# Performance work log

Hardware: AMD Instinct MI355X
Metric: run time of the kernel (lower is better)

Reference implementation:

```python
import jax, jax.numpy as jnp
import numpy as np
from math import ceil

N, C_IN, HV, WV = 4, 3, 256, 256
C, K, NUM_LAYERS = 16, 3, 10
HK, WK = 45, 45
PROX_SCALE, KSCALE, KBSCALE, EPS = 10.0, 100.0, 0.01, 1e-8


def conv2_same(x, w):
    # torch F.conv2d (cross-correlation) with 'same' padding
    return jax.lax.conv_general_dilated(x, w, (1, 1), 'SAME',
                                        dimension_numbers=('NCHW', 'OIHW', 'NCHW'))


def pad_to(x, size):
    h, w = x.shape[-2], x.shape[-1]
    pads = [(0, 0)] * (x.ndim - 2) + [(0, size[0] - h), (0, size[1] - w)]
    return jnp.pad(x, pads)


def soft_threshold(x, b):
    return jnp.sign(x) * jax.nn.relu(jnp.abs(x) - b)


def circ_shift(x, s):
    return jnp.roll(x, (-s[0], -s[1]), axis=(-2, -1))


def csq(c):
    return (c * jnp.conj(c)).real


def forward(blurred_image, w0, ws, biases, kernel_biases, kernel_proxes, zetas, eta):
    Nb, C_in, Hv, Wv = blurred_image.shape
    Hs, Ws = Hv + HK - 1, Wv + WK - 1
    Hb, Wb = Hs + HK - 1, Ws + WK - 1
    fft_size = (int(ceil(Hb / 64.0) * 64), int(ceil(Wb / 64.0) * 64))
    rfft = lambda x: jnp.fft.rfft2(x, s=fft_size, axes=(-2, -1))
    irfft = lambda X: jnp.fft.irfft2(X, s=fft_size, axes=(-2, -1))

    # first-layer filter: zero-mean per (out,in) filter, then spatial reflect
    w_mean = w0.reshape(C, C_in, -1).mean(axis=-1)
    w0c = w0 - w_mean[:, :, None, None]
    w0_unreflected = jnp.transpose(w0c, (1, 0, 2, 3))   # (C_in, C, K, K)
    w0r = w0c[:, :, ::-1, ::-1]

    # analysis: cascade of convs, each feature stack padded to fft_size
    wy_list = []
    fy = blurred_image
    for layer in range(NUM_LAYERS):
        w = w0r if layer == 0 else ws[layer - 1]
        fy = conv2_same(fy, w)
        fy_p = pad_to(jnp.pad(fy, ((0, 0), (0, 0), (HK - 1, HK - 1), (WK - 1, WK - 1))), fft_size)
        wy_list.append(fy_p)

    delta = jnp.zeros((Nb, HK, WK), dtype=blurred_image.dtype).at[:, HK // 2, WK // 2].set(1.0)
    b0 = biases[0][None, :, None, None]
    z = soft_threshold(circ_shift(wy_list[-1], (HK // 2, WK // 2)), b0)
    Fz = rfft(z)
    k = delta
    Fg = None
    for layer in range(NUM_LAYERS):
        fy_p = wy_list.pop()
        Ffy = rfft(fy_p)                       # (N, C, H, Wf) complex
        Fk = rfft(k)[:, None]                  # (N, 1, H, Wf)
        zeta = PROX_SCALE * zetas[layer][None, :, None, None]
        num = zeta * (jnp.conj(Fk) * Ffy) + Fz
        den = zeta * csq(Fk) + 1.0
        Fg = num / (den + EPS)
        b = biases[layer + 1][None, :, None, None]
        z = soft_threshold(irfft(Fg), b)
        Fz = rfft(z)
        zk = kernel_proxes[layer]
        num_k = zk * jnp.sum(jnp.conj(Fz) * Ffy, axis=1) + Fk[:, 0]
        den_k = zk * jnp.sum(csq(Fz), axis=1) + 1.0
        k = irfft(num_k / (den_k + EPS))
        k_flat = k.reshape(Nb, -1)
        k_max = jax.scipy.special.logsumexp(k_flat * KSCALE, axis=-1) / KSCALE
        bk = KBSCALE * kernel_biases[layer]
        k = jax.nn.relu(k[:, :HK, :WK] - bk * k_max[:, None, None])
        k_sum = jnp.sum(k, axis=(1, 2), keepdims=True)
        k = (k + EPS * delta) / (k_sum + EPS)

    # final closed-form image solve in frequency domain (3-channel Cramer's rule)
    Fy = rfft(jnp.pad(blurred_image, ((0, 0), (0, 0), (HK - 1, HK - 1), (WK - 1, WK - 1))))
    Fk = rfft(k)                                # (N, H, Wf)
    Fw0 = rfft(circ_shift(pad_to(w0_unreflected, fft_size), (K // 2, K // 2)))  # (C_in, C, H, Wf)
    b_final = biases[NUM_LAYERS + 1][None, :, None, None]
    Fg = rfft(soft_threshold(irfft(Fg), b_final))

    eta_s = PROX_SCALE * eta[None, :, None, None]      # (1, C, 1, 1)
    Fwr, Fwg, Fwb = Fw0[0:1], Fw0[1:2], Fw0[2:3]       # (1, C, H, Wf)
    Fyr, Fyg, Fyb = Fy[:, 0], Fy[:, 1], Fy[:, 2]
    Fk_sq = csq(Fk)
    Crr = Fk_sq + jnp.sum(eta_s * csq(Fwr), axis=1)
    Cgg = Fk_sq + jnp.sum(eta_s * csq(Fwg), axis=1)
    Cbb = Fk_sq + jnp.sum(eta_s * csq(Fwb), axis=1)
    Crg = jnp.sum(eta_s * jnp.conj(Fwr) * Fwg, axis=1)
    Crb = jnp.sum(eta_s * jnp.conj(Fwr) * Fwb, axis=1)
    Cgb = jnp.sum(eta_s * jnp.conj(Fwg) * Fwb, axis=1)
    Fk_conj = jnp.conj(Fk)
    Br = Fk_conj * Fyr + jnp.sum(eta_s * jnp.conj(Fwr) * Fg, axis=1)
    Bg = Fk_conj * Fyg + jnp.sum(eta_s * jnp.conj(Fwg) * Fg, axis=1)
    Bb = Fk_conj * Fyb + jnp.sum(eta_s * jnp.conj(Fwb) * Fg, axis=1)
    Crg_sq, Crb_sq, Cgb_sq = csq(Crg), csq(Crb), csq(Cgb)
    Irr = Cgg * Cbb - Cgb_sq
    Igg = Crr * Cbb - Crb_sq
    Ibb = Crr * Cgg - Crg_sq
    Irg = jnp.conj(Cgb) * Crb - Cbb * Crg
    Irb = Crg * Cgb - Cgg * Crb
    Igb = jnp.conj(Crg) * Crb - Crr * Cgb
    den = (Crr * (Cgg * Cbb - Cgb_sq) - Cgg * Crb_sq - Cbb * Crg_sq
           + 2 * (Crg * Cgb * jnp.conj(Crb)).real) + EPS
    Fxr = Irr * Br + Irg * Bg + Irb * Bb
    Fxg = jnp.conj(Irg) * Br + Igg * Bg + Igb * Bb
    Fxb = jnp.conj(Irb) * Br + jnp.conj(Igb) * Bg + Ibb * Bb
    Fx = jnp.stack([Fxr, Fxg, Fxb], axis=1) / den[:, None]

    image = irfft(Fx)[:, :, HK // 2:HK // 2 + Hv, WK // 2:WK // 2 + Wv]
    return image, k


def setup_inputs() -> dict:
    key = jax.random.key(0)
    ks = jax.random.split(key, 4)

    def xavier(k, shape, fan_in, fan_out):
        std = (2.0 / (fan_in + fan_out)) ** 0.5
        return std * jax.random.normal(k, shape, dtype=jnp.float32)

    return {
        'blurred_image': jax.random.normal(ks[0], (N, C_IN, HV, WV), dtype=jnp.float32),
        'w0': xavier(ks[1], (C, C_IN, K, K), C_IN * K * K, C * K * K),
        'ws': xavier(ks[2], (NUM_LAYERS - 1, C, C, 3, 3), C * 9, C * 9),
        'biases': jnp.full((NUM_LAYERS + 2, C), 0.02, dtype=jnp.float32),
        'kernel_biases': jnp.zeros((NUM_LAYERS,), dtype=jnp.float32),
        'kernel_proxes': jnp.ones((NUM_LAYERS,), dtype=jnp.float32),
        'zetas': jnp.ones((NUM_LAYERS, C), dtype=jnp.float32),
        'eta': jnp.ones((C,), dtype=jnp.float32),
    }


def reference(blurred_image, w0, ws, biases, kernel_biases, kernel_proxes, zetas, eta):
    return forward(blurred_image, w0, ws, biases, kernel_biases, kernel_proxes, zetas, eta)
```

## Files before the change

kernel.cpp:

```cpp
#include <hip/hip_runtime.h>
#include <math.h>

#define FH 384
#define KF 193
#define SPW 147456

typedef __attribute__((ext_vector_type(8))) short short8;
typedef __attribute__((ext_vector_type(4))) float f32x4;
typedef unsigned int u32;
typedef unsigned short u16;

static __device__ __forceinline__ float softt(float v, float b) {
    return copysignf(fmaxf(fabsf(v) - b, 0.f), v);
}
static __device__ __forceinline__ u16 bf16_rn(float v) {
    u32 u = __float_as_uint(v);
    u32 r = (u + 0x7FFFu + ((u >> 16) & 1u)) >> 16;
    return (u16)r;
}
static __device__ __forceinline__ float bf16_to_f(u16 h) {
    return __uint_as_float(((u32)h) << 16);
}
static __device__ __forceinline__ float2 ldc(const uint2* __restrict__ S, size_t i) {
    uint2 u = S[i];
    float2 r;
    r.x = __uint_as_float((u.x & 0xffffu) << 16) + __uint_as_float((u.y & 0xffffu) << 16);
    r.y = __uint_as_float(u.x & 0xffff0000u) + __uint_as_float(u.y & 0xffff0000u);
    return r;
}
static __device__ __forceinline__ float2 ldcu(uint2 u) {
    float2 r;
    r.x = __uint_as_float((u.x & 0xffffu) << 16) + __uint_as_float((u.y & 0xffffu) << 16);
    r.y = __uint_as_float(u.x & 0xffff0000u) + __uint_as_float(u.y & 0xffff0000u);
    return r;
}
static __device__ __forceinline__ uint2 packc(float re, float im) {
    u16 hr = bf16_rn(re), hi = bf16_rn(im);
    u16 lr = bf16_rn(re - bf16_to_f(hr)), li = bf16_rn(im - bf16_to_f(hi));
    uint2 o; o.x = (u32)hr | ((u32)hi << 16); o.y = (u32)lr | ((u32)li << 16);
    return o;
}
static __device__ __forceinline__ float2 cmul(float2 a, float2 b) {
    float2 r; r.x = a.x*b.x - a.y*b.y; r.y = a.x*b.y + a.y*b.x; return r;
}

__global__ void init_ef_k(float2* Ef) {
    int idx = blockIdx.x * 256 + threadIdx.x;
    if (idx >= FH * FH) return;
    int h = idx / FH, j = idx % FH;
    int m = (h * j) % FH;
    float th = (float)(6.283185307179586 / FH) * (float)m;
    float2 v; v.x = cosf(th); v.y = -sinf(th);
    Ef[idx] = v;
}

__global__ void init_tw(float2* twT) {
    int i = blockIdx.x * 256 + threadIdx.x;
    if (i < 384) {
        float th = (float)(6.283185307179586 / 384.0) * (float)i;
        float2 v; v.x = cosf(th); v.y = sinf(th);
        twT[i] = v;
    }
}

__global__ void init_e48(u16* __restrict__ H, u16* __restrict__ L, int inv)
{
    int idx = blockIdx.x * 256 + threadIdx.x;
    if (idx >= 96 * 96) return;
    int gm = idx / 96, kp = idx % 96;
    int m = gm >> 1, comp = gm & 1;
    int t = kp >> 1, ri = kp & 1;
    int mm = (m * t) % 48;
    float th = (float)(6.283185307179586 / 48.0) * (float)mm;
    float c = cosf(th), s = sinf(th);
    float er, ei;
    if (inv) { er = c * (1.f/384.f); ei = s * (1.f/384.f); }
    else     { er = c;               ei = -s; }
    float v;
    if (comp == 0) v = (ri == 0) ? er : -ei;
    else           v = (ri == 0) ? ei :  er;
    u16 h = bf16_rn(v);
    H[idx] = h;
    L[idx] = bf16_rn(v - bf16_to_f(h));
}

__global__ void init_t192(u16* __restrict__ H, u16* __restrict__ L)
{
    int idx = blockIdx.x * 256 + threadIdx.x;
    if (idx >= 208 * 192) return;
    int n = idx / 192, m = idx % 192;
    float v = 0.f;
    if (n < 194) {
        int j = n >> 1, ri = n & 1;
        int mm = (j * m) % 192;
        float th = (float)(6.283185307179586 / 192.0) * (float)mm;
        v = ri ? -sinf(th) : cosf(th);
    }
    u16 h = bf16_rn(v);
    H[idx] = h;
    L[idx] = bf16_rn(v - bf16_to_f(h));
}

__global__ void init_u192(u16* __restrict__ H, u16* __restrict__ L)
{
    int idx = blockIdx.x * 256 + threadIdx.x;
    if (idx >= 192 * 224) return;
    int m = idx / 224, kk = idx % 224;
    float v = 0.f;
    if (kk < 194) {
        int j = kk >> 1, ri = kk & 1;
        float cj = (j == 0 || j == 96) ? (1.f/384.f) : (2.f/384.f);
        int mm = (j * m) % 192;
        float th = (float)(6.283185307179586 / 192.0) * (float)mm;
        v = ri ? -cj*sinf(th) : cj*cosf(th);
    }
    u16 h = bf16_rn(v);
    H[idx] = h;
    L[idx] = bf16_rn(v - bf16_to_f(h));
}

__global__ void w0c_kernel(const float* __restrict__ w0, float* __restrict__ w0c) {
    int t = threadIdx.x;
    if (t < 48) {
        float m = 0.f;
        for (int d = 0; d < 9; ++d) m += w0[t*9+d];
        m *= (1.f/9.f);
        for (int d = 0; d < 9; ++d) w0c[t*9+d] = w0[t*9+d] - m;
    }
}

__global__ __launch_bounds__(256) void conv3x3_kernel(
    const float* __restrict__ inpF0, const u16* __restrict__ inH0, const u16* __restrict__ inL0,
    const float* __restrict__ w,
    u16* __restrict__ outH0, u16* __restrict__ outL0, int Cin, int flip,
    size_t inImgStride)
{
    size_t iofs = (size_t)blockIdx.z * inImgStride;
    const float* inF = inpF0 ? inpF0 + iofs : nullptr;
    const u16*   iH  = inH0 ? inH0 + iofs : nullptr;
    const u16*   iL  = inL0 ? inL0 + iofs : nullptr;
    u16* oH = outH0 + (size_t)blockIdx.z * 16*65536;
    u16* oL = outL0 + (size_t)blockIdx.z * 16*65536;
    __shared__ float tile[18][19];
    __shared__ float wl[16*16*9];
    int x0 = blockIdx.x * 16, y0 = blockIdx.y * 16;
    int t = threadIdx.x;
    int tx = t & 15, ty = t >> 4;
    int nw = 16 * Cin * 9;
    for (int i = t; i < nw; i += 256) {
        int d = i % 9;
        wl[i] = flip ? w[i + 8 - 2*d] : w[i];
    }
    float acc[16];
#pragma unroll
    for (int co = 0; co < 16; ++co) acc[co] = 0.f;
    for (int ci = 0; ci < Cin; ++ci) {
        __syncthreads();
        for (int i = t; i < 18*18; i += 256) {
            int yy = i / 18, xx = i % 18;
            int gy = y0 - 1 + yy, gx = x0 - 1 + xx;
            float v = 0.f;
            if (gy >= 0 && gy < 256 && gx >= 0 && gx < 256) {
                size_t ii;
                if (inF) ii = ((size_t)ci*256 + gy)*256 + gx;
                else     ii = ((size_t)ci*256 + gy)*256 + ((gx>>1) + (gx&1)*128);
                v = inF ? inF[ii] : (bf16_to_f(iH[ii]) + bf16_to_f(iL[ii]));
            }
            tile[yy][xx] = v;
        }
        __syncthreads();
        float v[9];
#pragma unroll
        for (int dy = 0; dy < 3; dy++)
#pragma unroll
            for (int dx = 0; dx < 3; dx++) v[dy*3+dx] = tile[ty+dy][tx+dx];
#pragma unroll
        for (int co = 0; co < 16; co++) {
            const float* wp = &wl[(co*Cin+ci)*9];
            acc[co] += v[0]*wp[0]+v[1]*wp[1]+v[2]*wp[2]
                     + v[3]*wp[3]+v[4]*wp[4]+v[5]*wp[5]
                     + v[6]*wp[6]+v[7]*wp[7]+v[8]*wp[8];
        }
    }
    int xo = x0 + tx;
    int xd = (xo >> 1) + (xo & 1)*128;
#pragma unroll
    for (int co = 0; co < 16; co++) {
        size_t o = ((size_t)co*256 + (y0+ty))*256 + xd;
        u16 h = bf16_rn(acc[co]);
        oH[o] = h;
        oL[o] = bf16_rn(acc[co] - bf16_to_f(h));
    }
}

__global__ void zinit_kernel(const u16* __restrict__ fy9H, const u16* __restrict__ fy9L,
                             const float* __restrict__ b0,
// ... 259 lines not shown
{
    int idx = blockIdx.x*256 + threadIdx.x;
    if (idx >= rows * 97) return;
    int j = idx % 97;
    size_t b = (size_t)(idx / 97) * KF;
    if (j == 96) {
        float2 f = ldc(S, b + 96);
        S[b + 96] = packc(2.f*f.x, -2.f*f.y);
    } else {
        float2 f1 = ldc(S, b + j);
        float2 f2 = ldc(S, b + 192 - j);
        float gpx = f1.x + f2.x, gpy = f1.y - f2.y;
        float hx  = f1.x - f2.x, hy  = f1.y + f2.y;
        float2 tw = twT[j];
        float gmx = tw.x*hx - tw.y*hy;
        float gmy = tw.x*hy + tw.y*hx;
        S[b + j]       = packc(gpx, gpy);
        S[b + 192 - j] = packc(gmx, gmy);
    }
}

template<bool FUSE_LSE>
__global__ __launch_bounds__(256) void c2r192(
    const uint2* __restrict__ Ain,
    const u16* __restrict__ UH, const u16* __restrict__ UL,
    float* __restrict__ outp, const float* __restrict__ thr,
    u16* __restrict__ spH, u16* __restrict__ spL, int B,
    float2* __restrict__ parts)
{
    __shared__ u16 AhS[2][8*64*8];
    __shared__ u16 AlS[2][8*64*8];
    int col0 = blockIdx.x * 64;
    int y0   = blockIdx.y * 128;
    int plane = blockIdx.z;
    int tid = threadIdx.x;
    int wave = tid >> 6, lane = tid & 63;
    int lm = lane & 15, lq = lane >> 4;
    f32x4 accP[2][4], accQ[2][4];
#pragma unroll
    for (int mi = 0; mi < 2; ++mi)
#pragma unroll
        for (int nj = 0; nj < 4; ++nj) {
            accP[mi][nj] = (f32x4){0.f,0.f,0.f,0.f};
            accQ[mi][nj] = (f32x4){0.f,0.f,0.f,0.f};
        }
    for (int kt = 0; kt < 194; kt += 32) {
#pragma unroll
        for (int s = 0; s < 8; ++s) {
            int slot = tid + s*256;
            int p   = slot >> 10;
            int inr = slot & 1023;
            int r = inr >> 3, kq = inr & 7;
            size_t rowb = ((size_t)(y0 + r)*B + plane)*KF;
            int j0 = (kt + kq*4) >> 1;
            uint2 u0, u1;
            u0.x = u0.y = u1.x = u1.y = 0u;
            if (p == 0) {
                if (j0 < 96) u0 = Ain[rowb + j0];
                else if (j0 == 96) {
                    uint2 t = Ain[rowb + 96];
                    u0.x = t.x & 0xffffu; u0.y = t.y & 0xffffu;
                }
                if (j0 + 1 < 96) u1 = Ain[rowb + j0 + 1];
            } else {
                if (j0 < 96) u0 = Ain[rowb + 192 - j0];
                else if (j0 == 96) {
                    uint2 t = Ain[rowb + 96];
                    u0.x = t.x >> 16; u0.y = t.y >> 16;
                }
                if (j0 + 1 < 96) u1 = Ain[rowb + 191 - j0];
            }
            int base = ((r >> 4)*64 + (r & 15) + 16*(kq >> 1))*8 + (kq & 1)*4;
            uint2 hp, lp;
            hp.x = u0.x; hp.y = u1.x;
            lp.x = u0.y; lp.y = u1.y;
            *(uint2*)&AhS[p][base] = hp;
            *(uint2*)&AlS[p][base] = lp;
        }
        __syncthreads();
        short8 A0h[2], A0l[2], A1h[2], A1l[2];
#pragma unroll
        for (int mi = 0; mi < 2; ++mi) {
            int fo = ((wave*2 + mi)*64 + lane)*8;
            A0h[mi] = *(const short8*)&AhS[0][fo];
            A0l[mi] = *(const short8*)&AlS[0][fo];
            A1h[mi] = *(const short8*)&AhS[1][fo];
            A1l[mi] = *(const short8*)&AlS[1][fo];
        }
#pragma unroll
        for (int nj = 0; nj < 4; ++nj) {
            size_t toff = (size_t)(col0 + nj*16 + lm)*224 + kt + lq*8;
            short8 Bh = *(const short8*)(UH + toff);
            short8 Bl = *(const short8*)(UL + toff);
#pragma unroll
            for (int mi = 0; mi < 2; ++mi) {
                accP[mi][nj] = __builtin_amdgcn_mfma_f32_16x16x32_bf16(A0h[mi], Bh, accP[mi][nj], 0, 0, 0);
                accP[mi][nj] = __builtin_amdgcn_mfma_f32_16x16x32_bf16(A0h[mi], Bl, accP[mi][nj], 0, 0, 0);
                accP[mi][nj] = __builtin_amdgcn_mfma_f32_16x16x32_bf16(A0l[mi], Bh, accP[mi][nj], 0, 0, 0);
                accQ[mi][nj] = __builtin_amdgcn_mfma_f32_16x16x32_bf16(A1h[mi], Bh, accQ[mi][nj], 0, 0, 0);
                accQ[mi][nj] = __builtin_amdgcn_mfma_f32_16x16x32_bf16(A1h[mi], Bl, accQ[mi][nj], 0, 0, 0);
                accQ[mi][nj] = __builtin_amdgcn_mfma_f32_16x16x32_bf16(A1l[mi], Bh, accQ[mi][nj], 0, 0, 0);
            }
        }
        __syncthreads();
    }
    float bthr = thr ? thr[plane & 15] : 0.f;
    float lm_ = -1e30f, ls_ = 0.f;
#pragma unroll
    for (int mi = 0; mi < 2; ++mi) {
#pragma unroll
        for (int nj = 0; nj < 4; ++nj) {
            int m = col0 + nj*16 + lm;
#pragma unroll
            for (int rr = 0; rr < 4; ++rr) {
                int y = y0 + wave*32 + mi*16 + lq*4 + rr;
                float xe = accP[mi][nj][rr];
                float xo = accQ[mi][nj][rr];
                float2 o2; o2.x = xe; o2.y = xo;
                *(float2*)&outp[((size_t)plane*FH + y)*FH + 2*m] = o2;
                if (spH) {
                    float s0 = softt(xe, bthr), s1 = softt(xo, bthr);
                    u16 h0 = bf16_rn(s0), h1 = bf16_rn(s1);
                    u16 l0 = bf16_rn(s0 - bf16_to_f(h0)), l1 = bf16_rn(s1 - bf16_to_f(h1));
                    size_t d = (size_t)plane*SPW + (size_t)y*FH + m;
                    spH[d]       = h0; spL[d]       = l0;
                    spH[d + 192] = h1; spL[d + 192] = l1;
                }
                if (FUSE_LSE) {
                    lse_comb(lm_, ls_, 100.f*xe, 1.f);
                    lse_comb(lm_, ls_, 100.f*xo, 1.f);
                }
            }
        }
    }
    if (FUSE_LSE) {
        __shared__ float sm[256], ss[256];
        sm[tid] = lm_; ss[tid] = ls_;
        __syncthreads();
        for (int st = 128; st > 0; st >>= 1) {
            if (tid < st) {
                float mm = sm[tid], sc = ss[tid];
                lse_comb(mm, sc, sm[tid+st], ss[tid+st]);
                sm[tid] = mm; ss[tid] = sc;
            }
            __syncthreads();
        }
        if (tid == 0) {
            float2 o; o.x = sm[0]; o.y = ss[0];
            parts[plane*9 + blockIdx.y*3 + blockIdx.x] = o;
        }
    }
}

template<bool FUSE_FG>
__global__ __launch_bounds__(384) void zgemm_col_mfma8(
    const u16* __restrict__ EH, const u16* __restrict__ EL,
    const uint2* __restrict__ Bm, uint2* __restrict__ Cm, int N, float sgn,
    int ktHi, const float2* __restrict__ twT,
    uint2* __restrict__ FzFg, const uint2* __restrict__ FkB,
    const float* __restrict__ zet16, int GKF)
{
    __shared__ u16 BhS[8][2*64*8];
    __shared__ u16 BlS[8][2*64*8];
    int col0 = blockIdx.x * 32;
    int tid = threadIdx.x;
    int wave = tid >> 6, lane = tid & 63;
    int lm = lane & 15, lq = lane >> 4;
    f32x4 acc[8][2];
#pragma unroll
    for (int p = 0; p < 8; ++p)
#pragma unroll
        for (int nj = 0; nj < 2; ++nj)
            acc[p][nj] = (f32x4){0.f,0.f,0.f,0.f};
    int arow = wave*16 + lm;
    for (int kt = 0; kt < ktHi; kt += 32) {
        int tbase = kt >> 1;
#pragma unroll
        for (int s = 0; s < 6; ++s) {
            int slot = tid + s*384;
            if (slot < 2048) {
                int p    = slot >> 8;
                int inr  = slot & 255;
                int pair = inr >> 5;
                int n    = inr & 31;
                int gn   = col0 + n;
                int t0   = tbase + pair*2;
                uint2 u0, u1;
                u0.x = u0.y = u1.x = u1.y = 0u;
                if (gn < N) {
                    u0 = Bm[(size_t)(8*t0 + p)*N + gn];
                    u1 = Bm[(size_t)(8*t0 + 8 + p)*N + gn];
                }
                int ntile = n >> 4, n0 = n & 15;
                int lrow  = (pair >> 1)*16 + n0;
                int base  = (ntile*64 + lrow)*8 + (pair & 1)*4;
                uint2 hp, lp;
                hp.x = u0.x; hp.y = u1.x;
                lp.x = u0.y; lp.y = u1.y;
                *(uint2*)&BhS[p][base] = hp;
                *(uint2*)&BlS[p][base] = lp;
            }
        }
        __syncthreads();
        short8 Ah, Al;
        {
            size_t aoff = (size_t)arow*96 + kt + lq*8;
            Ah = *(const short8*)(EH + aoff);
            Al = *(const short8*)(EL + aoff);
        }
#pragma unroll
        for (int nj = 0; nj < 2; ++nj) {
#pragma unroll
            for (int p = 0; p < 8; ++p) {
                short8 Bh = *(const short8*)&BhS[p][(nj*64 + lane)*8];
                short8 Bl = *(const short8*)&BlS[p][(nj*64 + lane)*8];
                acc[p][nj] = __builtin_amdgcn_mfma_f32_16x16x32_bf16(Ah, Bh, acc[p][nj], 0, 0, 0);
                acc[p][nj] = __builtin_amdgcn_mfma_f32_16x16x32_bf16(Ah, Bl, acc[p][nj], 0, 0, 0);
                acc[p][nj] = __builtin_amdgcn_mfma_f32_16x16x32_bf16(Al, Bh, acc[p][nj], 0, 0, 0);
            }
        }
        __syncthreads();
    }
    const float rt = 0.70710678118654752f;
#pragma unroll
    for (int nj = 0; nj < 2; ++nj) {
        int coln = col0 + nj*16 + lm;
        if (coln < N) {
            int r0 = wave*16 + lq*4;
            int h0b = r0 >> 1;
            int kk = 0, imgI = 0;
            float zeta = 0.f;
            if (FUSE_FG) {
                int planeI = coln / KF;
                kk = coln - planeI*KF;
                imgI = planeI >> 4;
                zeta = 10.f * zet16[planeI & 15];
            }
#pragma unroll
            for (int pp = 0; pp < 2; ++pp) {
                int h0 = h0b + pp;
                float2 d[8];
                d[0].x = acc[0][nj][2*pp]; d[0].y = acc[0][nj][2*pp+1];
#pragma unroll
                for (int p = 1; p < 8; ++p) {
                    float2 w = twT[p*h0];
                    w.y *= sgn;
                    float2 c; c.x = acc[p][nj][2*pp]; c.y = acc[p][nj][2*pp+1];
                    d[p] = cmul(c, w);
                }
                float2 e0, e1, e2, e3, o0, o1, o2, o3;
                e0.x = d[0].x + d[4].x; e0.y = d[0].y + d[4].y;
                e1.x = d[1].x + d[5].x; e1.y = d[1].y + d[5].y;
                e2.x = d[2].x + d[6].x; e2.y = d[2].y + d[6].y;
                e3.x = d[3].x + d[7].x; e3.y = d[3].y + d[7].y;
                o0.x = d[0].x - d[4].x; o0.y = d[0].y - d[4].y;
                o1.x = d[1].x - d[5].x; o1.y = d[1].y - d[5].y;
                o2.x = d[2].x - d[6].x; o2.y = d[2].y - d[6].y;
                o3.x = d[3].x - d[7].x; o3.y = d[3].y - d[7].y;
                float2 s02, m02, s13, m13, i13;
                s02.x = e0.x + e2.x; s02.y = e0.y + e2.y;
                m02.x = e0.x - e2.x; m02.y = e0.y - e2.y;
                s13.x = e1.x + e3.x; s13.y = e1.y + e3.y;
                m13.x = e1.x - e3.x; m13.y = e1.y - e3.y;
                i13.x = -sgn*m13.y;  i13.y = sgn*m13.x;
                float2 X[8];
                X[0].x = s02.x + s13.x; X[0].y = s02.y + s13.y;
                X[4].x = s02.x - s13.x; X[4].y = s02.y - s13.y;
                X[2].x = m02.x + i13.x; X[2].y = m02.y + i13.y;
                X[6].x = m02.x - i13.x; X[6].y = m02.y - i13.y;
                float2 g0 = o0, g1, g2, g3;
                g1.x = rt*(o1.x - sgn*o1.y);  g1.y = rt*(sgn*o1.x + o1.y);
                g2.x = -sgn*o2.y;             g2.y = sgn*o2.x;
                g3.x = rt*(-(o3.x + sgn*o3.y)); g3.y = rt*(sgn*o3.x - o3.y);
                float2 sp, mp, sq, mq, iq;
                sp.x = g0.x + g2.x; sp.y = g0.y + g2.y;
                mp.x = g0.x - g2.x; mp.y = g0.y - g2.y;
                sq.x = g1.x + g3.x; sq.y = g1.y + g3.y;
                mq.x = g1.x - g3.x; mq.y = g1.y - g3.y;
                iq.x = -sgn*mq.y;   iq.y = sgn*mq.x;
                X[1].x = sp.x + sq.x; X[1].y = sp.y + sq.y;
                X[5].x = sp.x - sq.x; X[5].y = sp.y - sq.y;
                X[3].x = mp.x + iq.x; X[3].y = mp.y + iq.y;
                X[7].x = mp.x - iq.x; X[7].y = mp.y - iq.y;
#pragma unroll
                for (int q = 0; q < 8; ++q) {
                    int row = h0 + 48*q;
                    uint2 px = packc(X[q].x, X[q].y);
                    Cm[(size_t)row*N + coln] = px;
                    if (FUSE_FG) {
                        float2 fy = ldcu(px);
                        float2 fz = ldc(FzFg, (size_t)row*N + coln);
                        float2 fk = ldc(FkB, (size_t)row*GKF + imgI*KF + kk);
                        float nx = zeta*(fk.x*fy.x + fk.y*fy.y) + fz.x;
                        float ny = zeta*(fk.x*fy.y - fk.y*fy.x) + fz.y;
                        float den = zeta*(fk.x*fk.x + fk.y*fk.y) + 1.f + 1e-8f;
                        float inv = 1.f/den;
                        FzFg[(size_t)row*N + coln] = packc(nx*inv, ny*inv);
                    }
                }
            }
        }
    }
}

__global__ void knum_kernel(const uint2* __restrict__ Fz, const uint2* __restrict__ Ffy,
                            const uint2* __restrict__ Fk, const float* __restrict__ kprox,
                            int L, int total, uint2* __restrict__ outk)
{
    int idx = blockIdx.x*256 + threadIdx.x;
    if (idx >= total) return;
    int k = idx % KF; int r = idx / KF;
    float zk = kprox[L];
    float s1x = 0.f, s1y = 0.f, s2 = 0.f;
    for (int c = 0; c < 16; ++c) {
        size_t bi = ((size_t)r*16 + c)*KF + k;
        float2 fz = ldc(Fz, bi), fy = ldc(Ffy, bi);
        s1x += fz.x*fy.x + fz.y*fy.y;
        s1y += fz.x*fy.y - fz.y*fy.x;
        s2  += fz.x*fz.x + fz.y*fz.y;
    }
    float2 fk = ldc(Fk, idx);
    float nx = zk*s1x + fk.x, ny = zk*s1y + fk.y;
    float den = zk*s2 + 1.f + 1e-8f;
    float inv = 1.f/den;
    outk[idx] = packc(nx*inv, ny*inv);
}

__global__ void zero_kernel(float* __restrict__ p, int n)
{
    int i = blockIdx.x*256 + threadIdx.x;
    if (i < n) p[i] = 0.f;
}

__global__ void kdelta_kernel(float* __restrict__ kful, int G)
{
    int t = threadIdx.x;
    if (t < G) kful[(size_t)t*FH*FH + 22*FH + 22] = 1.f;
}

__global__ __launch_bounds__(256) void knew_kernel(const float2* __restrict__ parts,
    const float* __restrict__ kraw0, const float* __restrict__ kb, int L,
    float* __restrict__ kful0)
{
    int img = blockIdx.x;
    const float* kraw = kraw0 + (size_t)img*FH*FH;
    float*       kful = kful0 + (size_t)img*FH*FH;
    int t = threadIdx.x;
    __shared__ float sm[16], ss[16];
    if (t < 16) {
        if (t < 9) { float2 p = parts[img*9 + t]; sm[t] = p.x; ss[t] = p.y; }
        else       { sm[t] = -1e30f; ss[t] = 0.f; }
    }
    __syncthreads();
    for (int st = 8; st > 0; st >>= 1) {
        if (t < st) {
            float mm = sm[t], sc = ss[t];
            lse_comb(mm, sc, sm[t+st], ss[t+st]);
            sm[t] = mm; ss[t] = sc;
        }
        __syncthreads();
    }
    float kmax = (sm[0] + logf(ss[0])) * 0.01f;
    float thr = 0.01f * kb[L] * kmax;
    float vs[8]; float loc = 0.f;
#pragma unroll
    for (int ii = 0; ii < 8; ++ii) {
        int i = t + ii*256;
        float v = 0.f;
        if (i < 45*45) {
            int y = i/45, x = i - y*45;
            v = fmaxf(kraw[y*FH + x] - thr, 0.f);
        }
        vs[ii] = v; loc += v;
    }
    __shared__ float sr[256];
    sr[t] = loc; __syncthreads();
    for (int st = 128; st > 0; st >>= 1) { if (t < st) sr[t] += sr[t+st]; __syncthreads(); }
    float den = sr[0] + 1e-8f;
#pragma unroll
    for (int ii = 0; ii < 8; ++ii) {
        int i = t + ii*256;
        if (i < 45*45) {
            int y = i/45, x = i - y*45;
            float v = vs[ii] + ((y == 22 && x == 22) ? 1e-8f : 0.f);
            kful[y*FH + x] = v / den;
        }
    }
}

__global__ void fw0_kernel(const float* __restrict__ w0c, const float2* __restrict__ Ef,
                           float2* __restrict__ Fw0)
{
    int idx = blockIdx.x*256 + threadIdx.x;
    if (idx >= 48*FH*KF) return;
    int k = idx % KF; int r = idx / KF;
    int c = r & 15; int r2 = r >> 4;
    int ci = r2 % 3; int h = r2 / 3;
    float accx = 0.f, accy = 0.f;
#pragma unroll
    for (int ky = 0; ky < 3; ++ky) {
        int a1 = ky - 1; if (a1 < 0) a1 += FH;
        float2 e1 = Ef[h*FH + a1];
#pragma unroll
        for (int kx = 0; kx < 3; ++kx) {
            int a2 = kx - 1; if (a2 < 0) a2 += FH;
            float2 e2 = Ef[k*FH + a2];
            float wv = w0c[((c*3 + ci)*3 + ky)*3 + kx];
            float tr = e1.x*e2.x - e1.y*e2.y;
            float ti = e1.x*e2.y + e1.y*e2.x;
            accx += wv*tr; accy += wv*ti;
        }
    }
    float2 o; o.x = accx; o.y = accy;
    Fw0[idx] = o;
}

__global__ void wiener_kernel(const uint2* __restrict__ Fk, const uint2* __restrict__ Fy,
    const float2* __restrict__ Fw0, const uint2* __restrict__ Fg2,
    const float* __restrict__ eta, int G, int total, uint2* __restrict__ Fx)
{
    int idx = blockIdx.x*256 + threadIdx.x;
    if (idx >= total) return;
    int k = idx % KF; int r = idx / KF;
    int h = r / G;
    float2 fk = ldc(Fk, idx);
    float fksq = fk.x*fk.x + fk.y*fk.y;
    float2 fyr = ldc(Fy, ((size_t)3*r + 0)*KF + k);
    float2 fyg = ldc(Fy, ((size_t)3*r + 1)*KF + k);
    float2 fyb = ldc(Fy, ((size_t)3*r + 2)*KF + k);
    float Crr = fksq, Cgg = fksq, Cbb = fksq;
    float2 Crg, Crb, Cgb;
    Crg.x = Crg.y = Crb.x = Crb.y = Cgb.x = Cgb.y = 0.f;
    float2 Br, Bg, Bb;
    Br.x = fk.x*fyr.x + fk.y*fyr.y; Br.y = fk.x*fyr.y - fk.y*fyr.x;
    Bg.x = fk.x*fyg.x + fk.y*fyg.y; Bg.y = fk.x*fyg.y - fk.y*fyg.x;
    Bb.x = fk.x*fyb.x + fk.y*fyb.y; Bb.y = fk.x*fyb.y - fk.y*fyb.x;
    for (int c = 0; c < 16; ++c) {
        float es = 10.f * eta[c];
        float2 wr = Fw0[((size_t)h*48 +  0 + c)*KF + k];
        float2 wg = Fw0[((size_t)h*48 + 16 + c)*KF + k];
        float2 wb = Fw0[((size_t)h*48 + 32 + c)*KF + k];
        float2 g  = ldc(Fg2, ((size_t)r*16 + c)*KF + k);
        Crr += es*(wr.x*wr.x + wr.y*wr.y);
        Cgg += es*(wg.x*wg.x + wg.y*wg.y);
        Cbb += es*(wb.x*wb.x + wb.y*wb.y);
        Crg.x += es*(wr.x*wg.x + wr.y*wg.y); Crg.y += es*(wr.x*wg.y - wr.y*wg.x);
        Crb.x += es*(wr.x*wb.x + wr.y*wb.y); Crb.y += es*(wr.x*wb.y - wr.y*wb.x);
        Cgb.x += es*(wg.x*wb.x + wg.y*wb.y); Cgb.y += es*(wg.x*wb.y - wg.y*wb.x);
        Br.x += es*(wr.x*g.x + wr.y*g.y); Br.y += es*(wr.x*g.y - wr.y*g.x);
        Bg.x += es*(wg.x*g.x + wg.y*g.y); Bg.y += es*(wg.x*g.y - wg.y*g.x);
        Bb.x += es*(wb.x*g.x + wb.y*g.y); Bb.y += es*(wb.x*g.y - wb.y*g.x);
    }
    float Crg_sq = Crg.x*Crg.x + Crg.y*Crg.y;
    float Crb_sq = Crb.x*Crb.x + Crb.y*Crb.y;
    float Cgb_sq = Cgb.x*Cgb.x + Cgb.y*Cgb.y;
    float Irr = Cgg*Cbb - Cgb_sq;
    float Igg = Crr*Cbb - Crb_sq;
    float Ibb = Crr*Cgg - Crg_sq;
    float2 Irg, Irb, Igb;
    Irg.x = (Cgb.x*Crb.x + Cgb.y*Crb.y) - Cbb*Crg.x;
    Irg.y = (Cgb.x*Crb.y - Cgb.y*Crb.x) - Cbb*Crg.y;
    Irb.x = (Crg.x*Cgb.x - Crg.y*Cgb.y) - Cgg*Crb.x;
    Irb.y = (Crg.x*Cgb.y + Crg.y*Cgb.x) - Cgg*Crb.y;
    Igb.x = (Crg.x*Crb.x + Crg.y*Crb.y) - Crr*Cgb.x;
    Igb.y = (Crg.x*Crb.y - Crg.y*Crb.x) - Crr*Cgb.y;
    float tx_ = Crg.x*Cgb.x - Crg.y*Cgb.y;
    float ty_ = Crg.x*Cgb.y + Crg.y*Cgb.x;
    float den = Crr*Irr - Cgg*Crb_sq - Cbb*Crg_sq + 2.f*(tx_*Crb.x + ty_*Crb.y) + 1e-8f;
    float inv = 1.f/den;
    float ox, oy;
    ox = (Irr*Br.x + (Irg.x*Bg.x - Irg.y*Bg.y) + (Irb.x*Bb.x - Irb.y*Bb.y))*inv;
    oy = (Irr*Br.y + (Irg.x*Bg.y + Irg.y*Bg.x) + (Irb.x*Bb.y + Irb.y*Bb.x))*inv;
    Fx[((size_t)3*r + 0)*KF + k] = packc(ox, oy);
    ox = ((Irg.x*Br.x + Irg.y*Br.y) + Igg*Bg.x + (Igb.x*Bb.x - Igb.y*Bb.y))*inv;
    oy = ((Irg.x*Br.y - Irg.y*Br.x) + Igg*Bg.y + (Igb.x*Bb.y + Igb.y*Bb.x))*inv;
    Fx[((size_t)3*r + 1)*KF + k] = packc(ox, oy);
    ox = ((Irb.x*Br.x + Irb.y*Br.y) + (Igb.x*Bg.x + Igb.y*Bg.y) + Ibb*Bb.x)*inv;
    oy = ((Irb.x*Br.y - Irb.y*Br.x) + (Igb.x*Bg.y - Igb.y*Bg.x) + Ibb*Bb.y)*inv;
    Fx[((size_t)3*r + 2)*KF + k] = packc(ox, oy);
}

__global__ void crop_kernel(const float* __restrict__ sp, float* __restrict__ outp, int total)
{
    int idx = blockIdx.x*256 + threadIdx.x;
    if (idx >= total) return;
    int x = idx & 255; int r = idx >> 8; int y = r & 255; int plane = r >> 8;
    outp[idx] = sp[((size_t)plane*FH + (y+22))*FH + (x+22)];
}

__global__ void kcopy_kernel(const float* __restrict__ kful, float* __restrict__ outp, int total)
{
    int idx = blockIdx.x*256 + threadIdx.x;
    if (idx >= total) return;
    int rem = idx % 2025; int img = idx / 2025;
    int x = rem % 45; int y = rem / 45;
    outp[idx] = kful[(size_t)img*FH*FH + y*FH + x];
}

extern "C" void kernel_launch(void* const* d_in, const int* in_sizes, int n_in,
                              void* d_out, int out_size, void* d_ws, size_t ws_size,
                              hipStream_t stream)
{
    (void)in_sizes; (void)n_in; (void)out_size;
    const float* blurred = (const float*)d_in[0];
    const float* w0      = (const float*)d_in[1];
    const float* wsw     = (const float*)d_in[2];
    const float* biases  = (const float*)d_in[3];
    const float* kbias   = (const float*)d_in[4];
    const float* kprox   = (const float*)d_in[5];
    const float* zetas   = (const float*)d_in[6];
    const float* eta     = (const float*)d_in[7];
    float* outp = (float*)d_out;

    auto al = [](size_t b) { return (b + 255) & ~(size_t)255; };
    auto need = [&](int G) -> size_t {
        size_t s = 0;
        s += al((size_t)FH*FH*8);
        s += al(384*8);
        s += 4*al((size_t)96*96*2);
        s += 2*al((size_t)208*192*2);
        s += 2*al((size_t)192*224*2);
        s += al(432*4);
        s += 2*al((size_t)10*G*16*65536*2);
        s += al((size_t)G*16*FH*FH*4);
        s += 2*al((size_t)G*16*SPW*2);
        s += 3*al((size_t)G*16*FH*KF*8);
        s += 4*al((size_t)G*FH*KF*8);
        s += 2*al((size_t)G*FH*FH*4);
        s += 2*al((size_t)G*3*FH*KF*8);
        s += al((size_t)G*64*8);
        return s;
    };
    int G = 4;
    while (G > 1 && need(G) > ws_size) G >>= 1;

    char* base = (char*)d_ws;
    size_t off = 0;
    auto alloc = [&](size_t bytes) -> void* {
        void* p = (void*)(base + off);
        off += (bytes + 255) & ~(size_t)255;
        return p;
    };
    float2* Ef   = (float2*)alloc((size_t)FH*FH*8);
    float2* twT  = (float2*)alloc(384*8);
    u16* EfH = (u16*)alloc((size_t)96*96*2);
    u16* EfL = (u16*)alloc((size_t)96*96*2);
    u16* EiH = (u16*)alloc((size_t)96*96*2);
    u16* EiL = (u16*)alloc((size_t)96*96*2);
    u16* T1H = (u16*)alloc((size_t)208*192*2);
    u16* T1L = (u16*)alloc((size_t)208*192*2);
    u16* U1H = (u16*)alloc((size_t)192*224*2);
    u16* U1L = (u16*)alloc((size_t)192*224*2);
    float*  w0cB = (float*)alloc(432*4);
    u16*    fyH  = (u16*)alloc((size_t)10*G*16*65536*2);
    u16*    fyL  = (u16*)alloc((size_t)10*G*16*65536*2);
    float*  zsp  = (float*)alloc((size_t)G*16*FH*FH*4);
    u16*    zspSH= (u16*)alloc((size_t)G*16*SPW*2);
    u16*    zspSL= (u16*)alloc((size_t)G*16*SPW*2);
    uint2*  mid  = (uint2*)alloc((size_t)G*16*FH*KF*8);
    uint2*  FzFg = (uint2*)alloc((size_t)G*16*FH*KF*8);
    uint2*  Ffy  = (uint2*)alloc((size_t)G*16*FH*KF*8);
    uint2*  Fk   = (uint2*)alloc((size_t)G*FH*KF*8);
    uint2*  kfA  = (uint2*)alloc((size_t)G*FH*KF*8);
    uint2*  kfB  = (uint2*)alloc((size_t)G*FH*KF*8);
    uint2*  kmid = (uint2*)alloc((size_t)G*FH*KF*8);
    float*  kraw = (float*)alloc((size_t)G*FH*FH*4);
    float*  kful = (float*)alloc((size_t)G*FH*FH*4);
    uint2*  FyB  = (uint2*)alloc((size_t)G*3*FH*KF*8);
    uint2*  FxB  = (uint2*)alloc((size_t)G*3*FH*KF*8);
    float2* lseP = (float2*)alloc((size_t)G*64*8);
    float2* Fw0B = (float2*)fyH;

    init_ef_k<<<(FH*FH+255)/256, 256, 0, stream>>>(Ef);
    init_tw<<<2, 256, 0, stream>>>(twT);
    init_e48<<<(96*96+255)/256, 256, 0, stream>>>(EfH, EfL, 0);
    init_e48<<<(96*96+255)/256, 256, 0, stream>>>(EiH, EiL, 1);
    init_t192<<<(208*192+255)/256, 256, 0, stream>>>(T1H, T1L);
    init_u192<<<(192*224+255)/256, 256, 0, stream>>>(U1H, U1L);
    w0c_kernel<<<1, 64, 0, stream>>>(w0, w0cB);

    auto zgf = [&](const uint2* Bm, uint2* Cm, int Ncols) {
        zgemm_col_mfma8<false><<<dim3((Ncols+31)/32), 384, 0, stream>>>(
            EfH, EfL, Bm, Cm, Ncols, -1.f, 96, twT, nullptr, nullptr, nullptr, 0);
    };
    auto zgi = [&](const uint2* Bm, uint2* Cm, int Ncols) {
        zgemm_col_mfma8<false><<<dim3((Ncols+31)/32), 384, 0, stream>>>(
            EiH, EiL, Bm, Cm, Ncols, 1.f, 96, twT, nullptr, nullptr, nullptr, 0);
    };
    auto r2c = [&](const float* inp, int inH, int inW, int oY, int oX,
                   const float* thr, uint2* o, int B) {
        r2c192_f<<<dim3(4, 3, B), 256, 0, stream>>>(
            inp, inH, inW, inW, (size_t)inH*inW, oY, oX, thr, T1H, T1L, twT, o, B);
    };
    auto r2cs = [&](const u16* Hs, const u16* Ls, int inH, int inW, int oY, int oX,
                    uint2* o, int B) {
        r2c192_s<<<dim3(4, 3, B), 256, 0, stream>>>(
            Hs, Ls, inH, inW, oY, oX, T1H, T1L, twT, o, B);
    };
    auto c2r = [&](uint2* Ain, float* o, int B,
                   const float* thr, u16* sH, u16* sL) {
        int rows = FH * B;
        gpm_kernel<<<(rows*97 + 255)/256, 256, 0, stream>>>(Ain, twT, rows);
        c2r192<false><<<dim3(3, 3, B), 256, 0, stream>>>(
            Ain, U1H, U1L, o, thr, sH, sL, B, nullptr);
    };
    auto c2rk = [&](uint2* Ain, float* o, int B, float2* parts) {
        int rows = FH * B;
        gpm_kernel<<<(rows*97 + 255)/256, 256, 0, stream>>>(Ain, twT, rows);
        c2r192<true><<<dim3(3, 3, B), 256, 0, stream>>>(
            Ain, U1H, U1L, o, nullptr, nullptr, nullptr, B, parts);
    };
    auto r2ck = [&]() {
        r2c192_f<<<dim3(4, 1, G), 256, 0, stream>>>(
            kful, 45, 45, FH, (size_t)FH*FH, 0, 0, nullptr, T1H, T1L, twT, kmid, G);
        zgemm_col_mfma8<false><<<dim3((G*KF+31)/32), 384, 0, stream>>>(
            EfH, EfL, kmid, Fk, G*KF, -1.f, 32, twT, nullptr, nullptr, nullptr, 0);
    };

    const size_t CKL = (size_t)G*16*65536;

    for (int g0 = 0; g0 < 4; g0 += G) {
        const float* img = blurred + (size_t)g0*3*65536;

        conv3x3_kernel<<<dim3(16,16,G), 256, 0, stream>>>(
            img, nullptr, nullptr, w0cB, fyH, fyL, 3, 1, (size_t)3*65536);
        for (int l = 1; l < 10; ++l)
            conv3x3_kernel<<<dim3(16,16,G), 256, 0, stream>>>(
                nullptr, fyH + (size_t)(l-1)*CKL, fyL + (size_t)(l-1)*CKL,
                wsw + (size_t)(l-1)*2304,
                fyH + (size_t)l*CKL, fyL + (size_t)l*CKL, 16, 0, (size_t)16*65536);

        int totZ = G*16*FH*FH;
        zinit_kernel<<<(totZ+255)/256, 256, 0, stream>>>(
            fyH + 9*CKL, fyL + 9*CKL, biases, zspSH, zspSL, totZ);
        r2cs(zspSH, zspSL, FH, FH, 0, 0, mid, G*16);
        zgf(mid, FzFg, G*16*KF);

        zero_kernel<<<(G*FH*FH+255)/256, 256, 0, stream>>>(kful, G*FH*FH);
        kdelta_kernel<<<1, 64, 0, stream>>>(kful, G);

        int totK = G*FH*KF;
        int NS = G*16*KF;
        for (int it = 0; it < 10; ++it) {
            int Lfy = 9 - it;
            r2ck();
            r2cs(fyH + (size_t)Lfy*CKL, fyL + (size_t)Lfy*CKL, 256, 256, 44, 44, mid, G*16);
            zgemm_col_mfma8<true><<<dim3((NS+31)/32), 384, 0, stream>>>(
                EfH, EfL, mid, Ffy, NS, -1.f, 96, twT,
                FzFg, Fk, zetas + it*16, G*KF);
            zgi(FzFg, mid, NS);
            c2r(mid, zsp, G*16, biases + (it+1)*16, zspSH, zspSL);
            r2cs(zspSH, zspSL, FH, FH, 0, 0, mid, G*16);
            zgf(mid, FzFg, NS);
            knum_kernel<<<(totK+255)/256, 256, 0, stream>>>(FzFg, Ffy, Fk, kprox, it, totK, kfA);
            zgi(kfA, kfB, G*KF);
            c2rk(kfB, kraw, G, lseP);
            knew_kernel<<<G, 256, 0, stream>>>(lseP, kraw, kbias, it, kful);
        }

        r2c(img, 256, 256, 44, 44, nullptr, mid, 3*G);
        zgf(mid, FyB, 3*G*KF);
        r2ck();
        r2c(zsp, FH, FH, 0, 0, biases + 11*16, mid, G*16);
        zgf(mid, FzFg, G*16*KF);
        fw0_kernel<<<(48*FH*KF+255)/256, 256, 0, stream>>>(w0cB, Ef, Fw0B);
        wiener_kernel<<<(totK+255)/256, 256, 0, stream>>>(Fk, FyB, Fw0B, FzFg, eta, G, totK, FxB);
        zgi(FxB, mid, 3*G*KF);
        c2r(mid, zsp, 3*G, nullptr, nullptr, nullptr);
        int totC = G*3*65536;
        crop_kernel<<<(totC+255)/256, 256, 0, stream>>>(zsp, outp + (size_t)g0*3*65536, totC);
        int totKC = G*2025;
        kcopy_kernel<<<(totKC+255)/256, 256, 0, stream>>>(kful, outp + 786432 + g0*2025, totKC);
    }
}
```

Baseline: 7.612 ms.

## Fuse forward column DFT, Fg update and inverse column DFT into one kernel

Adds zgemm_fg_inv, which performs the forward column DFT GEMM, computes the Fg proximal update in registers, and then runs the inverse column DFT GEMM on that result using shared memory. No intermediate FzFg write and reread or separate inverse launch is needed. This removes one kernel launch and a full round trip of the spectrum through global memory in each of the 10 iterations. The cost is extra register pressure from holding packed results (pg) plus a second accumulator set, which may lower occupancy. The butterfly is factored into a helper, bfly8.

```diff
diff --git a/kernel.cpp b/kernel.cpp
--- a/kernel.cpp
+++ b/kernel.cpp
@@ -42,6 +42,53 @@
 }
 static __device__ __forceinline__ float2 cmul(float2 a, float2 b) {
     float2 r; r.x = a.x*b.x - a.y*b.y; r.y = a.x*b.y + a.y*b.x; return r;
+}
+
+static __device__ __forceinline__ void bfly8(const float2 cc[8], int h0, float sgn,
+                                             const float2* __restrict__ twT, float2 X[8])
+{
+    const float rt = 0.70710678118654752f;
+    float2 d[8];
+    d[0] = cc[0];
+#pragma unroll
+    for (int p = 1; p < 8; ++p) {
+        float2 w = twT[p*h0];
+        w.y *= sgn;
+        d[p] = cmul(cc[p], w);
+    }
+    float2 e0, e1, e2, e3, o0, o1, o2, o3;
+    e0.x = d[0].x + d[4].x; e0.y = d[0].y + d[4].y;
+    e1.x = d[1].x + d[5].x; e1.y = d[1].y + d[5].y;
+    e2.x = d[2].x + d[6].x; e2.y = d[2].y + d[6].y;
+    e3.x = d[3].x + d[7].x; e3.y = d[3].y + d[7].y;
+    o0.x = d[0].x - d[4].x; o0.y = d[0].y - d[4].y;
+    o1.x = d[1].x - d[5].x; o1.y = d[1].y - d[5].y;
+    o2.x = d[2].x - d[6].x; o2.y = d[2].y - d[6].y;
+    o3.x = d[3].x - d[7].x; o3.y = d[3].y - d[7].y;
+    float2 s02, m02, s13, m13, i13;
+    s02.x = e0.x + e2.x; s02.y = e0.y + e2.y;
+    m02.x = e0.x - e2.x; m02.y = e0.y - e2.y;
+    s13.x = e1.x + e3.x; s13.y = e1.y + e3.y;
+    m13.x = e1.x - e3.x; m13.y = e1.y - e3.y;
+    i13.x = -sgn*m13.y;  i13.y = sgn*m13.x;
+    X[0].x = s02.x + s13.x; X[0].y = s02.y + s13.y;
+    X[4].x = s02.x - s13.x; X[4].y = s02.y - s13.y;
+    X[2].x = m02.x + i13.x; X[2].y = m02.y + i13.y;
+    X[6].x = m02.x - i13.x; X[6].y = m02.y - i13.y;
+    float2 g0 = o0, g1, g2, g3;
+    g1.x = rt*(o1.x - sgn*o1.y);  g1.y = rt*(sgn*o1.x + o1.y);
+    g2.x = -sgn*o2.y;             g2.y = sgn*o2.x;
+    g3.x = rt*(-(o3.x + sgn*o3.y)); g3.y = rt*(sgn*o3.x - o3.y);
+    float2 sp, mp, sq, mq, iq;
+    sp.x = g0.x + g2.x; sp.y = g0.y + g2.y;
+    mp.x = g0.x - g2.x; mp.y = g0.y - g2.y;
+    sq.x = g1.x + g3.x; sq.y = g1.y + g3.y;
+    mq.x = g1.x - g3.x; mq.y = g1.y - g3.y;
+    iq.x = -sgn*mq.y;   iq.y = sgn*mq.x;
+    X[1].x = sp.x + sq.x; X[1].y = sp.y + sq.y;
+    X[5].x = sp.x - sq.x; X[5].y = sp.y - sq.y;
+    X[3].x = mp.x + iq.x; X[3].y = mp.y + iq.y;
+    X[7].x = mp.x - iq.x; X[7].y = mp.y - iq.y;
 }
 
 __global__ void init_ef_k(float2* Ef) {
@@ -607,13 +654,10 @@
     }
 }
 
-template<bool FUSE_FG>
 __global__ __launch_bounds__(384) void zgemm_col_mfma8(
     const u16* __restrict__ EH, const u16* __restrict__ EL,
     const uint2* __restrict__ Bm, uint2* __restrict__ Cm, int N, float sgn,
-    int ktHi, const float2* __restrict__ twT,
-    uint2* __restrict__ FzFg, const uint2* __restrict__ FkB,
-    const float* __restrict__ zet16, int GKF)
+    int ktHi, const float2* __restrict__ twT)
 {
     __shared__ u16 BhS[8][2*64*8];
     __shared__ u16 BlS[8][2*64*8];
@@ -676,82 +720,210 @@
         }
         __syncthreads();
     }
-    const float rt = 0.70710678118654752f;
 #pragma unroll
     for (int nj = 0; nj < 2; ++nj) {
         int coln = col0 + nj*16 + lm;
         if (coln < N) {
             int r0 = wave*16 + lq*4;
             int h0b = r0 >> 1;
-            int kk = 0, imgI = 0;
-            float zeta = 0.f;
-            if (FUSE_FG) {
-                int planeI = coln / KF;
-                kk = coln - planeI*KF;
-                imgI = planeI >> 4;
-                zeta = 10.f * zet16[planeI & 15];
-            }
 #pragma unroll
             for (int pp = 0; pp < 2; ++pp) {
                 int h0 = h0b + pp;
-                float2 d[8];
-                d[0].x = acc[0][nj][2*pp]; d[0].y = acc[0][nj][2*pp+1];
-#pragma unroll
-                for (int p = 1; p < 8; ++p) {
-                    float2 w = twT[p*h0];
-                    w.y *= sgn;
-                    float2 c; c.x = acc[p][nj][2*pp]; c.y = acc[p][nj][2*pp+1];
-                    d[p] = cmul(c, w);
-                }
-                float2 e0, e1, e2, e3, o0, o1, o2, o3;
-                e0.x = d[0].x + d[4].x; e0.y = d[0].y + d[4].y;
-                e1.x = d[1].x + d[5].x; e1.y = d[1].y + d[5].y;
-                e2.x = d[2].x + d[6].x; e2.y = d[2].y + d[6].y;
-                e3.x = d[3].x + d[7].x; e3.y = d[3].y + d[7].y;
-                o0.x = d[0].x - d[4].x; o0.y = d[0].y - d[4].y;
-                o1.x = d[1].x - d[5].x; o1.y = d[1].y - d[5].y;
-                o2.x = d[2].x - d[6].x; o2.y = d[2].y - d[6].y;
-                o3.x = d[3].x - d[7].x; o3.y = d[3].y - d[7].y;
-                float2 s02, m02, s13, m13, i13;
-                s02.x = e0.x + e2.x; s02.y = e0.y + e2.y;
-                m02.x = e0.x - e2.x; m02.y = e0.y - e2.y;
-                s13.x = e1.x + e3.x; s13.y = e1.y + e3.y;
-                m13.x = e1.x - e3.x; m13.y = e1.y - e3.y;
-                i13.x = -sgn*m13.y;  i13.y = sgn*m13.x;
+                float2 cc[8];
+#pragma unroll
+                for (int p = 0; p < 8; ++p) {
+                    cc[p].x = acc[p][nj][2*pp]; cc[p].y = acc[p][nj][2*pp+1];
+                }
                 float2 X[8];
-                X[0].x = s02.x + s13.x; X[0].y = s02.y + s13.y;
-                X[4].x = s02.x - s13.x; X[4].y = s02.y - s13.y;
-                X[2].x = m02.x + i13.x; X[2].y = m02.y + i13.y;
-                X[6].x = m02.x - i13.x; X[6].y = m02.y - i13.y;
-                float2 g0 = o0, g1, g2, g3;
-                g1.x = rt*(o1.x - sgn*o1.y);  g1.y = rt*(sgn*o1.x + o1.y);
-                g2.x = -sgn*o2.y;             g2.y = sgn*o2.x;
-                g3.x = rt*(-(o3.x + sgn*o3.y)); g3.y = rt*(sgn*o3.x - o3.y);
-                float2 sp, mp, sq, mq, iq;
-                sp.x = g0.x + g2.x; sp.y = g0.y + g2.y;
-                mp.x = g0.x - g2.x; mp.y = g0.y - g2.y;
-                sq.x = g1.x + g3.x; sq.y = g1.y + g3.y;
-                mq.x = g1.x - g3.x; mq.y = g1.y - g3.y;
-                iq.x = -sgn*mq.y;   iq.y = sgn*mq.x;
-                X[1].x = sp.x + sq.x; X[1].y = sp.y + sq.y;
-                X[5].x = sp.x - sq.x; X[5].y = sp.y - sq.y;
-                X[3].x = mp.x + iq.x; X[3].y = mp.y + iq.y;
-                X[7].x = mp.x - iq.x; X[7].y = mp.y - iq.y;
+                bfly8(cc, h0, sgn, twT, X);
+#pragma unroll
+                for (int q = 0; q < 8; ++q) {
+                    int row = h0 + 48*q;
+                    Cm[(size_t)row*N + coln] = packc(X[q].x, X[q].y);
+                }
+            }
+        }
+    }
+}
+
+__global__ __launch_bounds__(384) void zgemm_fg_inv(
+    const u16* __restrict__ EH, const u16* __restrict__ EL,
+    const u16* __restrict__ IH, const u16* __restrict__ IL,
+    uint2* __restrict__ Bm, uint2* __restrict__ Ffy,
+    const uint2* __restrict__ FzB, const uint2* __restrict__ FkB,
+    const float* __restrict__ zet16, int N, int GKF,
+    const float2* __restrict__ twT)
+{
+    __shared__ u16 BhS[8][2*64*8];
+    __shared__ u16 BlS[8][2*64*8];
+    int col0 = blockIdx.x * 32;
+    int tid = threadIdx.x;
+    int wave = tid >> 6, lane = tid & 63;
+    int lm = lane & 15, lq = lane >> 4;
+    int arow = wave*16 + lm;
+    f32x4 acc[8][2];
+#pragma unroll
+    for (int p = 0; p < 8; ++p)
+#pragma unroll
+        for (int nj = 0; nj < 2; ++nj)
+            acc[p][nj] = (f32x4){0.f,0.f,0.f,0.f};
+    for (int kt = 0; kt < 96; kt += 32) {
+        int tbase = kt >> 1;
+#pragma unroll
+        for (int s = 0; s < 6; ++s) {
+            int slot = tid + s*384;
+            if (slot < 2048) {
+                int p    = slot >> 8;
+                int inr  = slot & 255;
+                int pair = inr >> 5;
+                int n    = inr & 31;
+                int gn   = col0 + n;
+                int t0   = tbase + pair*2;
+                uint2 u0, u1;
+                u0.x = u0.y = u1.x = u1.y = 0u;
+                if (gn < N) {
+                    u0 = Bm[(size_t)(8*t0 + p)*N + gn];
+                    u1 = Bm[(size_t)(8*t0 + 8 + p)*N + gn];
+                }
+                int ntile = n >> 4, n0 = n & 15;
+                int lrow  = (pair >> 1)*16 + n0;
+                int base  = (ntile*64 + lrow)*8 + (pair & 1)*4;
+                uint2 hp, lp;
+                hp.x = u0.x; hp.y = u1.x;
+                lp.x = u0.y; lp.y = u1.y;
+                *(uint2*)&BhS[p][base] = hp;
+                *(uint2*)&BlS[p][base] = lp;
+            }
+        }
+        __syncthreads();
+        short8 Ah, Al;
+        {
+            size_t aoff = (size_t)arow*96 + kt + lq*8;
+            Ah = *(const short8*)(EH + aoff);
+            Al = *(const short8*)(EL + aoff);
+        }
+#pragma unroll
+        for (int nj = 0; nj < 2; ++nj) {
+#pragma unroll
+            for (int p = 0; p < 8; ++p) {
+                short8 Bh = *(const short8*)&BhS[p][(nj*64 + lane)*8];
+                short8 Bl = *(const short8*)&BlS[p][(nj*64 + lane)*8];
+                acc[p][nj] = __builtin_amdgcn_mfma_f32_16x16x32_bf16(Ah, Bh, acc[p][nj], 0, 0, 0);
+                acc[p][nj] = __builtin_amdgcn_mfma_f32_16x16x32_bf16(Ah, Bl, acc[p][nj], 0, 0, 0);
+                acc[p][nj] = __builtin_amdgcn_mfma_f32_16x16x32_bf16(Al, Bh, acc[p][nj], 0, 0, 0);
+            }
+        }
+        __syncthreads();
+    }
+    int r0 = wave*16 + lq*4;
+    int h0b = r0 >> 1;
+    uint2 pg[2][2][8];
+#pragma unroll
+    for (int nj = 0; nj < 2; ++nj)
+#pragma unroll
+        for (int pp = 0; pp < 2; ++pp)
+#pragma unroll
+            for (int q = 0; q < 8; ++q) { pg[nj][pp][q].x = 0u; pg[nj][pp][q].y = 0u; }
+#pragma unroll
+    for (int nj = 0; nj < 2; ++nj) {
+        int coln = col0 + nj*16 + lm;
+        if (coln < N) {
+            int planeI = coln / KF;
+            int kk = coln - planeI*KF;
+            int imgI = planeI >> 4;
+            float zeta = 10.f * zet16[planeI & 15];
+#pragma unroll
+            for (int pp = 0; pp < 2; ++pp) {
+                int h0 = h0b + pp;
+                float2 cc[8];
+#pragma unroll
+                for (int p = 0; p < 8; ++p) {
+                    cc[p].x = acc[p][nj][2*pp]; cc[p].y = acc[p][nj][2*pp+1];
+                }
+                float2 X[8];
+                bfly8(cc, h0, -1.f, twT, X);
 #pragma unroll
                 for (int q = 0; q < 8; ++q) {
                     int row = h0 + 48*q;
                     uint2 px = packc(X[q].x, X[q].y);
-                    Cm[(size_t)row*N + coln] = px;
-                    if (FUSE_FG) {
-                        float2 fy = ldcu(px);
-                        float2 fz = ldc(FzFg, (size_t)row*N + coln);
-                        float2 fk = ldc(FkB, (size_t)row*GKF + imgI*KF + kk);
-                        float nx = zeta*(fk.x*fy.x + fk.y*fy.y) + fz.x;
-                        float ny = zeta*(fk.x*fy.y - fk.y*fy.x) + fz.y;
-                        float den = zeta*(fk.x*fk.x + fk.y*fk.y) + 1.f + 1e-8f;
-                        float inv = 1.f/den;
-                        FzFg[(size_t)row*N + coln] = packc(nx*inv, ny*inv);
+                    Ffy[(size_t)row*N + coln] = px;
+                    float2 fy = ldcu(px);
+                    float2 fz = ldc(FzB, (size_t)row*N + coln);
+                    float2 fk = ldc(FkB, (size_t)row*GKF + imgI*KF + kk);
+                    float nx = zeta*(fk.x*fy.x + fk.y*fy.y) + fz.x;
+                    float ny = zeta*(fk.x*fy.y - fk.y*fy.x) + fz.y;
+                    float den = zeta*(fk.x*fk.x + fk.y*fk.y) + 1.f + 1e-8f;
+                    float inv = 1.f/den;
+                    pg[nj][pp][q] = packc(nx*inv, ny*inv);
+                }
+            }
+        }
+    }
+    f32x4 iacc[8][2];
+#pragma unroll
+    for (int p = 0; p < 8; ++p)
+#pragma unroll
+        for (int nj = 0; nj < 2; ++nj)
+            iacc[p][nj] = (f32x4){0.f,0.f,0.f,0.f};
+    for (int s = 0; s < 3; ++s) {
+        __syncthreads();
+#pragma unroll
+        for (int nj = 0; nj < 2; ++nj) {
+#pragma unroll
+            for (int pp = 0; pp < 2; ++pp) {
+                int h0 = h0b + pp;
+                int dd = h0 >> 3;
+                int p  = h0 & 7;
+#pragma unroll
+                for (int q = 0; q < 8; ++q) {
+                    int t = 6*q + dd;
+                    if ((t >> 4) == s) {
+                        int pair = (t >> 1) & 7;
+                        int off  = t & 1;
+                        int idx  = (nj*64 + (pair>>1)*16 + lm)*4 + (pair&1)*2 + off;
+                        ((u32*)BhS[p])[idx] = pg[nj][pp][q].x;
+                        ((u32*)BlS[p])[idx] = pg[nj][pp][q].y;
                     }
+                }
+            }
+        }
+        __syncthreads();
+        short8 Ah, Al;
+        {
+            size_t aoff = (size_t)arow*96 + 32*s + lq*8;
+            Ah = *(const short8*)(IH + aoff);
+            Al = *(const short8*)(IL + aoff);
+        }
+#pragma unroll
+        for (int nj = 0; nj < 2; ++nj) {
+#pragma unroll
+            for (int p = 0; p < 8; ++p) {
+                short8 Bh = *(const short8*)&BhS[p][(nj*64 + lane)*8];
+                short8 Bl = *(const short8*)&BlS[p][(nj*64 + lane)*8];
+                iacc[p][nj] = __builtin_amdgcn_mfma_f32_16x16x32_bf16(Ah, Bh, iacc[p][nj], 0, 0, 0);
+                iacc[p][nj] = __builtin_amdgcn_mfma_f32_16x16x32_bf16(Ah, Bl, iacc[p][nj], 0, 0, 0);
+                iacc[p][nj] = __builtin_amdgcn_mfma_f32_16x16x32_bf16(Al, Bh, iacc[p][nj], 0, 0, 0);
+            }
+        }
+    }
+#pragma unroll
+    for (int nj = 0; nj < 2; ++nj) {
+        int coln = col0 + nj*16 + lm;
+        if (coln < N) {
+#pragma unroll
+            for (int pp = 0; pp < 2; ++pp) {
+                int h0 = h0b + pp;
+                float2 cc[8];
+#pragma unroll
+                for (int p = 0; p < 8; ++p) {
+                    cc[p].x = iacc[p][nj][2*pp]; cc[p].y = iacc[p][nj][2*pp+1];
+                }
+                float2 X[8];
+                bfly8(cc, h0, 1.f, twT, X);
+#pragma unroll
+                for (int q = 0; q < 8; ++q) {
+                    int row = h0 + 48*q;
+                    Bm[(size_t)row*N + coln] = packc(X[q].x, X[q].y);
                 }
             }
         }
@@ -1035,12 +1207,12 @@
     w0c_kernel<<<1, 64, 0, stream>>>(w0, w0cB);
 
     auto zgf = [&](const uint2* Bm, uint2* Cm, int Ncols) {
-        zgemm_col_mfma8<false><<<dim3((Ncols+31)/32), 384, 0, stream>>>(
-            EfH, EfL, Bm, Cm, Ncols, -1.f, 96, twT, nullptr, nullptr, nullptr, 0);
+        zgemm_col_mfma8<<<dim3((Ncols+31)/32), 384, 0, stream>>>(
+            EfH, EfL, Bm, Cm, Ncols, -1.f, 96, twT);
     };
     auto zgi = [&](const uint2* Bm, uint2* Cm, int Ncols) {
-        zgemm_col_mfma8<false><<<dim3((Ncols+31)/32), 384, 0, stream>>>(
-            EiH, EiL, Bm, Cm, Ncols, 1.f, 96, twT, nullptr, nullptr, nullptr, 0);
+        zgemm_col_mfma8<<<dim3((Ncols+31)/32), 384, 0, stream>>>(
+            EiH, EiL, Bm, Cm, Ncols, 1.f, 96, twT);
     };
     auto r2c = [&](const float* inp, int inH, int inW, int oY, int oX,
                    const float* thr, uint2* o, int B) {
@@ -1068,8 +1240,8 @@
     auto r2ck = [&]() {
         r2c192_f<<<dim3(4, 1, G), 256, 0, stream>>>(
             kful, 45, 45, FH, (size_t)FH*FH, 0, 0, nullptr, T1H, T1L, twT, kmid, G);
-        zgemm_col_mfma8<false><<<dim3((G*KF+31)/32), 384, 0, stream>>>(
-            EfH, EfL, kmid, Fk, G*KF, -1.f, 32, twT, nullptr, nullptr, nullptr, 0);
+        zgemm_col_mfma8<<<dim3((G*KF+31)/32), 384, 0, stream>>>(
+            EfH, EfL, kmid, Fk, G*KF, -1.f, 32, twT);
     };
 
     const size_t CKL = (size_t)G*16*65536;
@@ -1100,10 +1272,8 @@
             int Lfy = 9 - it;
             r2ck();
             r2cs(fyH + (size_t)Lfy*CKL, fyL + (size_t)Lfy*CKL, 256, 256, 44, 44, mid, G*16);
-            zgemm_col_mfma8<true><<<dim3((NS+31)/32), 384, 0, stream>>>(
-                EfH, EfL, mid, Ffy, NS, -1.f, 96, twT,
-                FzFg, Fk, zetas + it*16, G*KF);
-            zgi(FzFg, mid, NS);
+            zgemm_fg_inv<<<dim3((NS+31)/32), 384, 0, stream>>>(
+                EfH, EfL, EiH, EiL, mid, Ffy, FzFg, Fk, zetas + it*16, NS, G*KF, twT);
             c2r(mid, zsp, G*16, biases + (it+1)*16, zspSH, zspSL);
             r2cs(zspSH, zspSL, FH, FH, 0, 0, mid, G*16);
             zgf(mid, FzFg, NS);
```

After: 7.376 ms (median of 2 runs). -3.1%, faster.
